# Performance work log

Hardware: AMD Instinct MI355X
Metric: run time of the kernel (lower is better)

Reference implementation:

```python
import jax, jax.numpy as jnp
import numpy as np

N_NODES = 50000
IN_NF = 64
HID = 128
OUT_NF = 64
EDGE_HID = HID // 2  # edge_nf_ratio = 2
N_LAYERS = 4
N_EDGES = 800000
NUM_LATENT_NODES = 64
C_EVEN = 1.0
C_ODD = 2.0 / NUM_LATENT_NODES


def setup_inputs() -> dict:
    key = jax.random.key(0)
    ks = jax.random.split(key, 24)
    def lin(k, fan_in, fan_out):
        # torch nn.Linear default init: U(-1/sqrt(fan_in), 1/sqrt(fan_in))
        bound = 1.0 / np.sqrt(fan_in)
        kw, kb = jax.random.split(k)
        w = jax.random.uniform(kw, (fan_in, fan_out), jnp.float32, -bound, bound)
        b = jax.random.uniform(kb, (fan_out,), jnp.float32, -bound, bound)
        return w, b

    h = jax.random.normal(ks[0], (N_NODES, IN_NF), jnp.float32)
    edges_a = jax.random.randint(ks[1], (2, N_EDGES), 0, N_NODES, jnp.int32)
    edges_b = jax.random.randint(ks[2], (2, N_EDGES), 0, N_NODES, jnp.int32)
    update_mask_a = jax.random.randint(ks[3], (N_NODES, 1), 0, 2, jnp.int32).astype(bool)
    update_mask_b = jax.random.randint(ks[4], (N_NODES, 1), 0, 2, jnp.int32).astype(bool)

    emb_in_w, emb_in_b = lin(ks[5], IN_NF, HID)
    emb_out_w, emb_out_b = lin(ks[6], HID, OUT_NF)

    ew1, eb1, ew2, eb2 = [], [], [], []
    nw1, nb1, nw2, nb2 = [], [], [], []
    for i in range(N_LAYERS):
        w, b = lin(ks[7 + i], 2 * HID, EDGE_HID); ew1.append(w); eb1.append(b)
        w, b = lin(ks[11 + i], EDGE_HID, EDGE_HID); ew2.append(w); eb2.append(b)
        w, b = lin(ks[15 + i], HID + EDGE_HID, HID); nw1.append(w); nb1.append(b)
        w, b = lin(ks[19 + i], HID, HID); nw2.append(w); nb2.append(b)

    stack = lambda xs: jnp.stack(xs, 0)
    return {
        "h": h, "edges_a": edges_a, "edges_b": edges_b,
        "update_mask_a": update_mask_a, "update_mask_b": update_mask_b,
        "emb_in_w": emb_in_w, "emb_in_b": emb_in_b,
        "emb_out_w": emb_out_w, "emb_out_b": emb_out_b,
        "edge_w1": stack(ew1), "edge_b1": stack(eb1),
        "edge_w2": stack(ew2), "edge_b2": stack(eb2),
        "node_w1": stack(nw1), "node_b1": stack(nb1),
        "node_w2": stack(nw2), "node_b2": stack(nb2),
    }


def _gcl(h, edges, mask, C, ew1, eb1, ew2, eb2, nw1, nb1, nw2, nb2):
    row, col = edges[0], edges[1]
    # edge model: gather source/target node feats -> 2-layer SiLU MLP
    feat = jnp.concatenate([h[row], h[col]], axis=-1)      # [E, 2*HID]
    m = jax.nn.silu(feat @ ew1 + eb1)                      # [E, EDGE_HID]
    m = jax.nn.silu(m @ ew2 + eb2)                         # [E, EDGE_HID]
    # aggregate messages to receiving nodes (scatter-add), scaled by C
    agg = jax.ops.segment_sum(m, row, num_segments=h.shape[0]) * C
    # node model with residual
    upd = jax.nn.silu(jnp.concatenate([h, agg], axis=-1) @ nw1 + nb1) @ nw2 + nb2
    h_new = h + upd
    # masked asynchronous update: only nodes with mask=True are updated
    return jnp.where(mask, h_new, h)


def reference(h, edges_a, edges_b, update_mask_a, update_mask_b,
              emb_in_w, emb_in_b, emb_out_w, emb_out_b,
              edge_w1, edge_b1, edge_w2, edge_b2,
              node_w1, node_b1, node_w2, node_b2):
    h = h @ emb_in_w + emb_in_b
    for i in range(N_LAYERS):
        if i % 2 == 0:
            edges, mask, C = edges_a, update_mask_a, C_EVEN
        else:
            edges, mask, C = edges_b, update_mask_b, C_ODD
        h = _gcl(h, edges, mask, C,
                 edge_w1[i], edge_b1[i], edge_w2[i], edge_b2[i],
                 node_w1[i], node_b1[i], node_w2[i], node_b2[i])
    h = h @ emb_out_w + emb_out_b
    return h
```

## Files before the change

kernel.cpp:

```cpp
#include <hip/hip_runtime.h>
#include <cstdint>

typedef __bf16 bf16_t;
typedef bf16_t bf16x8 __attribute__((ext_vector_type(8)));
typedef float floatx4 __attribute__((ext_vector_type(4)));
typedef unsigned short ushort4v __attribute__((ext_vector_type(4)));

constexpr int N_NODES = 50000;
constexpr int N_EDGES = 800000;
constexpr int HID = 128;
constexpr int EH = 64;
constexpr int NCH = (N_NODES + 255) / 256;

__device__ __forceinline__ float silu_f(float x) {
    return x * __builtin_amdgcn_rcpf(1.0f + __expf(-x));
}

__global__ __launch_bounds__(256) void pack_all_kernel(
    const float* __restrict__ embin, const float* __restrict__ embout,
    const float* __restrict__ ew1, const float* __restrict__ ew2,
    const float* __restrict__ nw1, const float* __restrict__ nw2,
    bf16_t* __restrict__ pk)
{
    int t = blockIdx.x * 256 + threadIdx.x;
    if (t >= 32768) {
        t -= 32768;
        int lane = t & 63, chunk = t >> 6;
        int ks = chunk & 3, nt = (chunk >> 2) & 7, l = chunk >> 5;
        int quad = lane >> 4, coln = lane & 15;
        const float* Wl = ew1 + l * 256 * 64;
        int kb = (nt >= 4 ? 128 : 0) + ks * 32 + quad * 8;
        int nc = (nt & 3) * 16 + coln;
        bf16x8 v;
#pragma unroll
        for (int j = 0; j < 8; j++) v[j] = (bf16_t)Wl[(kb + j) * 64 + nc];
        *(bf16x8*)(pk + 262144 + t * 8) = v;
        return;
    }
    const float* W; int K, Nc; int base; bf16_t* out;
    if (t < 1024)       { W = embin;  K = 64;  Nc = 128; base = 0;     out = pk; }
    else if (t < 2048)  { W = embout; K = 128; Nc = 64;  base = 1024;  out = pk + 8192; }
    else if (t < 10240) { W = ew1;    K = 256; Nc = 64;  base = 2048;  out = pk + 16384; }
    else if (t < 12288) { W = ew2;    K = 64;  Nc = 64;  base = 10240; out = pk + 81920; }
    else if (t < 24576) { W = nw1;    K = 192; Nc = 128; base = 12288; out = pk + 98304; }
    else                { W = nw2;    K = 128; Nc = 128; base = 24576; out = pk + 196608; }
    t -= base;
    int KS = K >> 5, NT = Nc >> 4;
    int lane = t & 63;
    int chunk = t >> 6;
    int ks = chunk % KS;
    int nt = (chunk / KS) % NT;
    int l  = chunk / (KS * NT);
    int quad = lane >> 4, coln = lane & 15;
    const float* Wl = W + l * K * Nc;
    bf16x8 v;
#pragma unroll
    for (int j = 0; j < 8; j++)
        v[j] = (bf16_t)Wl[(ks * 32 + quad * 8 + j) * Nc + nt * 16 + coln];
    *(bf16x8*)(out + t * 8) = v;
}

__global__ void hist2_kernel(const int* __restrict__ ea, const int* __restrict__ eb,
                             const int* __restrict__ ma, const int* __restrict__ mb,
                             int* __restrict__ ba, int* __restrict__ bb) {
    int half = gridDim.x >> 1;
    int b = blockIdx.x;
    const int* erows; const int* mask; int* bins;
    if (b < half) { erows = ea; mask = ma; bins = ba; }
    else          { erows = eb; mask = mb; bins = bb; b -= half; }
    int i = b * 256 + threadIdx.x;
    if (i >= N_EDGES) return;
    int r = erows[i];
    if (mask[r] != 0) atomicAdd(&bins[r], 1);
}

__global__ __launch_bounds__(256) void scan_phase1(
    const int* __restrict__ bins_a, const int* __restrict__ bins_b,
    int* __restrict__ bs_a, int* __restrict__ bs_b) {
    const int* bins = blockIdx.y ? bins_b : bins_a;
    int* bs = blockIdx.y ? bs_b : bs_a;
    int i = blockIdx.x * 256 + threadIdx.x;
    int v = (i < N_NODES) ? (bins[i] != 0 ? bins[i] : 0) : 0;
#pragma unroll
    for (int off = 32; off; off >>= 1) v += __shfl_down(v, off, 64);
    __shared__ int ws_[4];
    int lane = threadIdx.x & 63, wv = threadIdx.x >> 6;
    if (lane == 0) ws_[wv] = v;
    __syncthreads();
    if (threadIdx.x == 0) bs[blockIdx.x] = ws_[0] + ws_[1] + ws_[2] + ws_[3];
}

__global__ __launch_bounds__(256) void scan_phase2(
    int* __restrict__ bs_a, int* __restrict__ bs_b,
    int* __restrict__ bins_a, int* __restrict__ bins_b) {
    int* bs = blockIdx.x ? bs_b : bs_a;
    int* bins = blockIdx.x ? bins_b : bins_a;
    int t = threadIdx.x, lane = t & 63, wv = t >> 6;
    int v = (t < NCH) ? bs[t] : 0;
    int s = v;
#pragma unroll
    for (int off = 1; off < 64; off <<= 1) {
        int u = __shfl_up(s, off, 64);
        if (lane >= off) s += u;
    }
    __shared__ int wsum[4];
    if (lane == 63) wsum[wv] = s;
    __syncthreads();
    int woff = 0;
    for (int w = 0; w < wv; w++) woff += wsum[w];
    int excl = s - v + woff;
    if (t < NCH) bs[t] = excl;
    if (t == NCH - 1) bins[N_NODES] = excl + v;
}

__global__ __launch_bounds__(256) void mask_scan2(
    int* __restrict__ ms_a, int* __restrict__ ms_b,
    int* __restrict__ cnt_a, int* __restrict__ cnt_b) {
    int* ms = blockIdx.x ? ms_b : ms_a;
    int* cnt = blockIdx.x ? cnt_b : cnt_a;
    int t = threadIdx.x, lane = t & 63, wv = t >> 6;
    int v = (t < NCH) ? ms[t] : 0;
    int s = v;
#pragma unroll
    for (int off = 1; off < 64; off <<= 1) {
        int u = __shfl_up(s, off, 64);
        if (lane >= off) s += u;
    }
    __shared__ int wsum[4];
    if (lane == 63) wsum[wv] = s;
    __syncthreads();
    int woff = 0;
    for (int w = 0; w < wv; w++) woff += wsum[w];
    int excl = s - v + woff;
    if (t < NCH) ms[t] = excl;
    if (t == NCH - 1) cnt[0] = excl + v;
}

__global__ __launch_bounds__(256) void compact_kernel(
    const int* __restrict__ ma, const int* __restrict__ mb,
    const int* __restrict__ ms_a, const int* __restrict__ ms_b,
    int* __restrict__ la, int* __restrict__ lb) {
    const int* mask = blockIdx.y ? mb : ma;
    const int* ms = blockIdx.y ? ms_b : ms_a;
    int* list = blockIdx.y ? lb : la;
    int i = blockIdx.x * 256 + threadIdx.x;
    int t = threadIdx.x, lane = t & 63, wv = t >> 6;
    int m = (i < N_NODES) ? (mask[i] != 0) : 0;
    unsigned long long bal = __ballot(m != 0);
    int pos = (int)__popcll(bal & ((1ull << lane) - 1ull));
    __shared__ int wsum[4];
    if (lane == 63) wsum[wv] = pos + m;
    __syncthreads();
    int woff = 0;
    for (int w = 0; w < wv; w++) woff += wsum[w];
    if (m) list[ms[blockIdx.x] + woff + pos] = i;
}

__global__ __launch_bounds__(256) void scan_phase3(
    int* __restrict__ bins_a, int* __restrict__ bins_b,
    const int* __restrict__ bs_a, const int* __restrict__ bs_b) {
    int* bins = blockIdx.y ? bins_b : bins_a;
    const int* bs = blockIdx.y ? bs_b : bs_a;
    int i = blockIdx.x * 256 + threadIdx.x;
    int t = threadIdx.x, lane = t & 63, wv = t >> 6;
    int v = (i < N_NODES) ? bins[i] : 0;
    int s = v;
#pragma unroll
    for (int off = 1; off < 64; off <<= 1) {
        int u = __shfl_up(s, off, 64);
        if (lane >= off) s += u;
    }
    __shared__ int wsum[4];
    if (lane == 63) wsum[wv] = s;
    __syncthreads();
    int woff = 0;
    for (int w = 0; w < wv; w++) woff += wsum[w];
    if (i < N_NODES) bins[i] = s - v + woff + bs[blockIdx.x];
}

__global__ void fill_src_kernel(const int* __restrict__ bins_a, const int* __restrict__ bins_b,
                                int* __restrict__ ssrc_a, int* __restrict__ ssrc_b) {
    const int* bins = blockIdx.y ? bins_b : bins_a;
    int* ssrc = blockIdx.y ? ssrc_b : ssrc_a;
    int r = blockIdx.x * 256 + threadIdx.x;
    if (r >= N_NODES) return;
    int p0 = bins[r], p1 = bins[r + 1];
    for (int p = p0; p < p1; p++) ssrc[p] = r;
}

__global__ void scatter2_kernel(const int* __restrict__ ea, const int* __restrict__ eb,
                                const int* __restrict__ ma, const int* __restrict__ mb,
                                int* __restrict__ ba, int* __restrict__ bb,
                                int* __restrict__ sdst_a, int* __restrict__ sdst_b) {
    int half = gridDim.x >> 1;
    int b = blockIdx.x;
    const int* e; const int* mask; int* bins; int* sdst;
    if (b < half) { e = ea; mask = ma; bins = ba; sdst = sdst_a; }
    else          { e = eb; mask = mb; bins = bb; sdst = sdst_b; b -= half; }
    int i = b * 256 + threadIdx.x;
    if (i >= N_EDGES) return;
    int r = e[i];
    if (mask[r] == 0) return;
    int c = e[N_EDGES + i];
    int pos = atomicAdd(&bins[r], 1);
    sdst[pos] = c;
}

__global__ __launch_bounds__(256) void emb_in_kernel(
    const float* __restrict__ h0, const bf16_t* __restrict__ wp,
    const float* __restrict__ bias, float* __restrict__ h, bf16_t* __restrict__ h_bf)
{
    int t = threadIdx.x, wave = t >> 6, lane = t & 63;
    int quad = lane >> 4, col = lane & 15;
    int m0 = blockIdx.x * 64 + wave * 16;
    int ndc = min(m0 + col, N_NODES - 1);
    floatx4 acc[8] = {};
#pragma unroll
    for (int ks = 0; ks < 2; ks++) {
        const float* ap = h0 + ndc * 64 + ks * 32 + quad * 8;
        floatx4 f0 = *(const floatx4*)ap;
        floatx4 f1 = *(const floatx4*)(ap + 4);
        bf16x8 a;
#pragma unroll
        for (int j = 0; j < 4; j++) { a[j] = (bf16_t)f0[j]; a[j + 4] = (bf16_t)f1[j]; }
#pragma unroll
        for (int nt = 0; nt < 8; nt++) {
            bf16x8 b = ((const bf16x8*)wp)[(nt * 2 + ks) * 64 + lane];
            acc[nt] = __builtin_amdgcn_mfma_f32_16x16x32_bf16(a, b, acc[nt], 0, 0, 0);
        }
    }
#pragma unroll
    for (int r = 0; r < 4; r++) {
        int nd2 = m0 + quad * 4 + r;
        if (nd2 < N_NODES) {
#pragma unroll
            for (int nt = 0; nt < 8; nt++) {
                int n = nt * 16 + col;
                float x = acc[nt][r] + bias[n];
                h[nd2 * HID + n] = x;
                h_bf[nd2 * HID + n] = (bf16_t)x;
            }
        }
    }
}

__global__ __launch_bounds__(256) void pre_edge_kernel(
    const bf16_t* __restrict__ h_bf, const bf16_t* __restrict__ w1cat,
    const float* __restrict__ b1, float* __restrict__ P)
{
    int t = threadIdx.x, wave = t >> 6, lane = t & 63;
    int quad = lane >> 4, col = lane & 15;
    int m0 = blockIdx.x * 64 + wave * 16;
    int ndc = min(m0 + col, N_NODES - 1);
    floatx4 acc[8] = {};
#pragma unroll
    for (int ks = 0; ks < 4; ks++) {
        bf16x8 a = *(const bf16x8*)(h_bf + ndc * HID + ks * 32 + quad * 8);
#pragma unroll
        for (int nt = 0; nt < 8; nt++) {
            bf16x8 b = ((const bf16x8*)w1cat)[(nt * 4 + ks) * 64 + lane];
            acc[nt] = __builtin_amdgcn_mfma_f32_16x16x32_bf16(a, b, acc[nt], 0, 0, 0);
        }
    }
#pragma unroll
    for (int r = 0; r < 4; r++) {
        int nd2 = m0 + quad * 4 + r;
        if (nd2 < N_NODES) {
#pragma unroll
            for (int nt = 0; nt < 8; nt++) {
                int n = nt * 16 + col;
                float x = acc[nt][r] + (nt >= 4 ? b1[n - 64] : 0.0f);
                P[nd2 * 128 + n] = x;
            }
        }
    }
}

__global__ __launch_bounds__(256, 4) void edge_kernel_pre(
    const float* __restrict__ P, const int* __restrict__ ssrc,
    const int* __restrict__ sdst, const int* __restrict__ m_ptr,
    const bf16_t* __restrict__ w2p, const float* __restrict__ b2,
    float* __restrict__ agg, float C)
{
    __shared__ __align__(16) bf16_t pool[4][64 * 40];

    int t = threadIdx.x;
    int wave = t >> 6, lane = t & 63, quad = lane >> 4, col = lane & 15;
    bf16_t* mbT = pool[wave];

    float b2v[4];
#pragma unroll
    for (int nt = 0; nt < 4; nt++) b2v[nt] = b2[nt * 16 + col];

    int M = m_ptr[0];
    int ntiles = (M + 31) >> 5;
    int wid = blockIdx.x * 4 + wave, nw = gridDim.x * 4;
    if (wid >= ntiles) return;

    int sr = 0x7fffffff, ds = 0x7fffffff;
    { int p = wid * 32 + lane; if (lane < 32 && p < M) { sr = ssrc[p]; ds = sdst[p]; } }

    for (int tile = wid; tile < ntiles; tile += nw) {
        int tnc = min(tile + nw, ntiles - 1);
        int srn = 0x7fffffff, dsn = 0x7fffffff;
        { int p = tnc * 32 + lane; if (lane < 32 && p < M) { srn = ssrc[p]; dsn = sdst[p]; } }

        floatx4 acc2[2][4] = {};
#pragma unroll
        for (int m = 0; m < 2; m++) {
            int rN = min(__shfl(sr, m * 16 + col, 64), N_NODES - 1);
            int cN = min(__shfl(ds, m * 16 + col, 64), N_NODES - 1);
            const float* pr = P + rN * 128 + quad * 8;
            const float* pc = P + cN * 128 + 64 + quad * 8;
            floatx4 fr[4], fc[4];
#pragma unroll
            for (int ks = 0; ks < 2; ks++) {
                fr[ks * 2]     = *(const floatx4*)(pr + ks * 32);
                fr[ks * 2 + 1] = *(const floatx4*)(pr + ks * 32 + 4);
                fc[ks * 2]     = *(const floatx4*)(pc + ks * 32);
                fc[ks * 2 + 1] = *(const floatx4*)(pc + ks * 32 + 4);
            }
#pragma unroll
            for (int ks = 0; ks < 2; ks++) {
                bf16x8 a2;
#pragma unroll
                for (int j = 0; j < 4; j++) {
                    a2[j]     = (bf16_t)silu_f(fr[ks * 2][j]     + fc[ks * 2][j]);
                    a2[j + 4] = (bf16_t)silu_f(fr[ks * 2 + 1][j] + fc[ks * 2 + 1][j]);
                }
#pragma unroll
                for (int nt = 0; nt < 4; nt++) {
                    bf16x8 b = ((const bf16x8*)w2p)[(nt * 2 + ks) * 64 + lane];
                    acc2[m][nt] = __builtin_amdgcn_mfma_f32_16x16x32_bf16(a2, b, acc2[m][nt], 0, 0, 0);
                }
            }
        }

#pragma unroll
        for (int m = 0; m < 2; m++)
#pragma unroll
            for (int nt = 0; nt < 4; nt++) {
                ushort4v pv;
#pragma unroll
                for (int r = 0; r < 4; r++) {
                    bf16_t bv = (bf16_t)(silu_f(acc2[m][nt][r] + b2v[nt]) * C);
                    pv[r] = __builtin_bit_cast(unsigned short, bv);
                }
                *(ushort4v*)(mbT + (nt * 16 + col) * 40 + m * 16 + quad * 4) = pv;
            }

        {
            float mv[32];
#pragma unroll
            for (int i = 0; i < 4; i++) {
                bf16x8 v8 = *(const bf16x8*)(mbT + lane * 40 + i * 8);
#pragma unroll
                for (int j = 0; j < 8; j++) mv[i * 8 + j] = (float)v8[j];
            }
            int dp = __shfl(sr, 0, 64);
            float run = mv[0];
#pragma unroll
            for (int r = 1; r < 32; r++) {
                int d = __shfl(sr, r, 64);
                if (d != dp) {
                    if (dp < N_NODES) atomicAdd(agg + dp * EH + lane, run);
                    run = mv[r]; dp = d;
                } else run += mv[r];
            }
            if (dp < N_NODES) atomicAdd(agg + dp * EH + lane, run);
        }

        sr = srn; ds = dsn;
    }
}

__global__ __launch_bounds__(256, 3) void edge_kernel_sorted(
    const bf16_t* __restrict__ h_bf, const int* __restrict__ ssrc,
    const int* __restrict__ sdst, const int* __restrict__ m_ptr,
    const bf16_t* __restrict__ w1p, const float* __restrict__ b1,
    const bf16_t* __restrict__ w2p, const float* __restrict__ b2,
    float* __restrict__ agg, float C)
{
    __shared__ __align__(16) bf16_t w1s[16384];
    __shared__ __align__(16) bf16_t pool[4][64 * 40];

    int t = threadIdx.x;
#pragma unroll
    for (int i = 0; i < 8; i++)
        ((bf16x8*)w1s)[t + 256 * i] = ((const bf16x8*)w1p)[t + 256 * i];
    __syncthreads();

    int wave = t >> 6, lane = t & 63, quad = lane >> 4, col = lane & 15;
    bf16_t* hl = pool[wave];
    bf16_t* mbT = pool[wave];

    float b1v[4], b2v[4];
#pragma unroll
    for (int nt = 0; nt < 4; nt++) { b1v[nt] = b1[nt * 16 + col]; b2v[nt] = b2[nt * 16 + col]; }

    int M = m_ptr[0];
    int ntiles = (M + 31) >> 5;
    int wid = blockIdx.x * 4 + wave, nw = gridDim.x * 4;
    if (wid >= ntiles) return;

    int sr = 0x7fffffff, ds = 0x7fffffff;
    { int p = wid * 32 + lane; if (lane < 32 && p < M) { sr = ssrc[p]; ds = sdst[p]; } }
    bf16x8 a[2][8];
    {
        int ns0 = min(__shfl(sr, col, 64), N_NODES - 1);
        int ns1 = min(__shfl(sr, 16 + col, 64), N_NODES - 1);
        int nd0 = min(__shfl(ds, col, 64), N_NODES - 1);
        int nd1 = min(__shfl(ds, 16 + col, 64), N_NODES - 1);
#pragma unroll
        for (int ks = 0; ks < 8; ks++) {
            int o = (ks & 3) * 32 + quad * 8;
            a[0][ks] = *(const bf16x8*)(h_bf + (ks < 4 ? ns0 : nd0) * HID + o);
            a[1][ks] = *(const bf16x8*)(h_bf + (ks < 4 ? ns1 : nd1) * HID + o);
        }
    }

    for (int tile = wid; tile < ntiles; tile += nw) {
        int tnc = min(tile + nw, ntiles - 1);
        int srn = 0x7fffffff, dsn = 0x7fffffff;
        { int p = tnc * 32 + lane; if (lane < 32 && p < M) { srn = ssrc[p]; dsn = sdst[p]; } }

        floatx4 acc[2][4] = {};
#pragma unroll
        for (int ks = 0; ks < 8; ks++) {
#pragma unroll
            for (int nt = 0; nt < 4; nt++) {
                bf16x8 b = ((const bf16x8*)w1s)[(nt * 8 + ks) * 64 + lane];
                acc[0][nt] = __builtin_amdgcn_mfma_f32_16x16x32_bf16(a[0][ks], b, acc[0][nt], 0, 0, 0);
                acc[1][nt] = __builtin_amdgcn_mfma_f32_16x16x32_bf16(a[1][ks], b, acc[1][nt], 0, 0, 0);
            }
        }

        bf16x8 an[2][8];
        {
            int ns0 = min(__shfl(srn, col, 64), N_NODES - 1);
            int ns1 = min(__shfl(srn, 16 + col, 64), N_NODES - 1);
            int nd0 = min(__shfl(dsn, col, 64), N_NODES - 1);
            int nd1 = min(__shfl(dsn, 16 + col, 64), N_NODES - 1);
#pragma unroll
            for (int ks = 0; ks < 8; ks++) {
                int o = (ks & 3) * 32 + quad * 8;
                an[0][ks] = *(const bf16x8*)(h_bf + (ks < 4 ? ns0 : nd0) * HID + o);
                an[1][ks] = *(const bf16x8*)(h_bf + (ks < 4 ? ns1 : nd1) * HID + o);
            }
        }

#pragma unroll
        for (int m = 0; m < 2; m++)
#pragma unroll
            for (int nt = 0; nt < 4; nt++)
#pragma unroll
                for (int r = 0; r < 4; r++)
                    hl[(m * 16 + quad * 4 + r) * 72 + nt * 16 + col] =
                        (bf16_t)silu_f(acc[m][nt][r] + b1v[nt]);

        floatx4 acc2[2][4] = {};
#pragma unroll
        for (int ks = 0; ks < 2; ks++) {
            bf16x8 a2[2];
#pragma unroll
            for (int m = 0; m < 2; m++)
                a2[m] = *(const bf16x8*)(hl + (m * 16 + col) * 72 + ks * 32 + quad * 8);
#pragma unroll
            for (int nt = 0; nt < 4; nt++) {
                bf16x8 b = ((const bf16x8*)w2p)[(nt * 2 + ks) * 64 + lane];
                acc2[0][nt] = __builtin_amdgcn_mfma_f32_16x16x32_bf16(a2[0], b, acc2[0][nt], 0, 0, 0);
                acc2[1][nt] = __builtin_amdgcn_mfma_f32_16x16x32_bf16(a2[1], b, acc2[1][nt], 0, 0, 0);
            }
        }
#pragma unroll
        for (int m = 0; m < 2; m++)
#pragma unroll
            for (int nt = 0; nt < 4; nt++) {
                ushort4v p;
#pragma unroll
                for (int r = 0; r < 4; r++) {
                    bf16_t bv = (bf16_t)(silu_f(acc2[m][nt][r] + b2v[nt]) * C);
                    p[r] = __builtin_bit_cast(unsigned short, bv);
                }
                *(ushort4v*)(mbT + (nt * 16 + col) * 40 + m * 16 + quad * 4) = p;
            }

        {
            float mv[32];
#pragma unroll
            for (int i = 0; i < 4; i++) {
                bf16x8 v8 = *(const bf16x8*)(mbT + lane * 40 + i * 8);
#pragma unroll
                for (int j = 0; j < 8; j++) mv[i * 8 + j] = (float)v8[j];
            }
            int dp = __shfl(sr, 0, 64);
            float run = mv[0];
#pragma unroll
            for (int r = 1; r < 32; r++) {
                int d = __shfl(sr, r, 64);
                if (d != dp) {
                    if (dp < N_NODES) atomicAdd(agg + dp * EH + lane, run);
                    run = mv[r]; dp = d;
                } else run += mv[r];
            }
            if (dp < N_NODES) atomicAdd(agg + dp * EH + lane, run);
        }

        sr = srn; ds = dsn;
#pragma unroll
        for (int m = 0; m < 2; m++)
#pragma unroll
            for (int ks = 0; ks < 8; ks++) a[m][ks] = an[m][ks];
    }
}

__global__ __launch_bounds__(256) void edge_kernel(
    const bf16_t* __restrict__ h_bf, const int* __restrict__ edges,
    const int* __restrict__ mask,
    const bf16_t* __restrict__ w1p, const float* __restrict__ b1,
    const bf16_t* __restrict__ w2p, const float* __restrict__ b2,
    float* __restrict__ agg, float C)
{
    __shared__ __align__(16) bf16_t w1s[16384];
    __shared__ __align__(16) bf16_t w2s[4096];
    __shared__ __align__(16) bf16_t hl[4][16 * 72];

    int t = threadIdx.x;
#pragma unroll
    for (int i = 0; i < 8; i++)
        ((bf16x8*)w1s)[t + 256 * i] = ((const bf16x8*)w1p)[t + 256 * i];
#pragma unroll
    for (int i = 0; i < 2; i++)
        ((bf16x8*)w2s)[t + 256 * i] = ((const bf16x8*)w2p)[t + 256 * i];
    __syncthreads();

    int wave = t >> 6, lane = t & 63, quad = lane >> 4, col = lane & 15;
    bf16_t* myhl = hl[wave];

    float b1v[4], b2v[4];
#pragma unroll
    for (int nt = 0; nt < 4; nt++) { b1v[nt] = b1[nt * 16 + col]; b2v[nt] = b2[nt * 16 + col]; }

    const int ntile_cnt = N_EDGES / 64;
    for (int tile = blockIdx.x; tile < ntile_cnt; tile += gridDim.x) {
        int ebase = tile * 64 + wave * 16;
        int src = edges[ebase + col];
        int dst = edges[N_EDGES + ebase + col];

        floatx4 acc[4] = {};
#pragma unroll
        for (int ks = 0; ks < 8; ks++) {
            int idx = (ks < 4) ? src : dst;
            bf16x8 a = *(const bf16x8*)(h_bf + idx * HID + (ks & 3) * 32 + quad * 8);
#pragma unroll
            for (int nt = 0; nt < 4; nt++) {
                bf16x8 b = ((const bf16x8*)w1s)[(nt * 8 + ks) * 64 + lane];
                acc[nt] = __builtin_amdgcn_mfma_f32_16x16x32_bf16(a, b, acc[nt], 0, 0, 0);
            }
        }
#pragma unroll
        for (int nt = 0; nt < 4; nt++)
#pragma unroll
            for (int r = 0; r < 4; r++)
                myhl[(quad * 4 + r) * 72 + nt * 16 + col] = (bf16_t)silu_f(acc[nt][r] + b1v[nt]);
        __syncthreads();

        floatx4 acc2[4] = {};
#pragma unroll
        for (int ks = 0; ks < 2; ks++) {
            bf16x8 a = *(const bf16x8*)(myhl + col * 72 + ks * 32 + quad * 8);
#pragma unroll
            for (int nt = 0; nt < 4; nt++) {
                bf16x8 b = ((const bf16x8*)w2s)[(nt * 2 + ks) * 64 + lane];
                acc2[nt] = __builtin_amdgcn_mfma_f32_16x16x32_bf16(a, b, acc2[nt], 0, 0, 0);
            }
        }
#pragma unroll
        for (int r = 0; r < 4; r++) {
            int dest = edges[ebase + quad * 4 + r];
            if (mask[dest] != 0) {
                float* aggp = agg + dest * EH;
#pragma unroll
                for (int nt = 0; nt < 4; nt++) {
                    float x = acc2[nt][r] + b2v[nt];
                    atomicAdd(aggp + nt * 16 + col, silu_f(x) * C);
                }
            }
        }
        __syncthreads();
    }
}

__global__ __launch_bounds__(256) void node_kernel_masked(
    float* __restrict__ h, bf16_t* __restrict__ h_bf,
    float* __restrict__ agg, const int* __restrict__ list,
    const int* __restrict__ cnt_ptr,
    const bf16_t* __restrict__ w1p, const float* __restrict__ b1,
    const bf16_t* __restrict__ w2p, const float* __restrict__ b2)
{
    __shared__ __align__(16) bf16_t hl[4][16 * 136];
    int t = threadIdx.x, wave = t >> 6, lane = t & 63;
    int quad = lane >> 4, col = lane & 15;
    int cnt = cnt_ptr[0];
    int m0 = blockIdx.x * 64 + wave * 16;
    if (m0 >= cnt) return;
    int lv = list[min(m0 + col, cnt - 1)];
    int ndc = lv;

    floatx4 acc[8] = {};
#pragma unroll
    for (int ks = 0; ks < 6; ks++) {
        bf16x8 a;
        if (ks < 4) {
            a = *(const bf16x8*)(h_bf + ndc * HID + ks * 32 + quad * 8);
        } else {
            const float* ap = agg + ndc * EH + (ks - 4) * 32 + quad * 8;
            floatx4 f0 = *(const floatx4*)ap;
            floatx4 f1 = *(const floatx4*)(ap + 4);
#pragma unroll
            for (int j = 0; j < 4; j++) { a[j] = (bf16_t)f0[j]; a[j + 4] = (bf16_t)f1[j]; }
        }
#pragma unroll
        for (int nt = 0; nt < 8; nt++) {
            bf16x8 b = ((const bf16x8*)w1p)[(nt * 6 + ks) * 64 + lane];
            acc[nt] = __builtin_amdgcn_mfma_f32_16x16x32_bf16(a, b, acc[nt], 0, 0, 0);
        }
    }
    if ((m0 + col) < cnt) {
        floatx4 z = {0.0f, 0.0f, 0.0f, 0.0f};
        float* zp = agg + ndc * EH + quad * 8;
        *(floatx4*)zp = z; *(floatx4*)(zp + 4) = z;
        *(floatx4*)(zp + 32) = z; *(floatx4*)(zp + 36) = z;
    }
    bf16_t* myhl = hl[wave];
#pragma unroll
    for (int nt = 0; nt < 8; nt++)
#pragma unroll
        for (int r = 0; r < 4; r++) {
            float x = acc[nt][r] + b1[nt * 16 + col];
            myhl[(quad * 4 + r) * 136 + nt * 16 + col] = (bf16_t)silu_f(x);
        }

    floatx4 acc2[8] = {};
#pragma unroll
    for (int ks = 0; ks < 4; ks++) {
        bf16x8 a = *(const bf16x8*)(myhl + col * 136 + ks * 32 + quad * 8);
#pragma unroll
        for (int nt = 0; nt < 8; nt++) {
            bf16x8 b = ((const bf16x8*)w2p)[(nt * 4 + ks) * 64 + lane];
            acc2[nt] = __builtin_amdgcn_mfma_f32_16x16x32_bf16(a, b, acc2[nt], 0, 0, 0);
        }
    }
#pragma unroll
    for (int r = 0; r < 4; r++) {
        if ((m0 + quad * 4 + r) < cnt) {
            int nd2 = __shfl(lv, quad * 4 + r, 64);
#pragma unroll
            for (int nt = 0; nt < 8; nt++) {
                int n = nt * 16 + col;
                float hv = h[nd2 * HID + n] + acc2[nt][r] + b2[n];
                h[nd2 * HID + n] = hv;
                h_bf[nd2 * HID + n] = (bf16_t)hv;
            }
        }
    }
}

__global__ __launch_bounds__(256) void node_kernel(
    float* __restrict__ h, bf16_t* __restrict__ h_bf,
    float* __restrict__ agg, const int* __restrict__ mask,
    const bf16_t* __restrict__ w1p, const float* __restrict__ b1,
    const bf16_t* __restrict__ w2p, const float* __restrict__ b2,
    const bf16_t* __restrict__ wop, const float* __restrict__ bo,
    float* __restrict__ out)
{
    __shared__ __align__(16) bf16_t hl[4][16 * 136];
    int t = threadIdx.x, wave = t >> 6, lane = t & 63;
    int quad = lane >> 4, col = lane & 15;
    int m0 = blockIdx.x * 64 + wave * 16;
    int ndc = min(m0 + col, N_NODES - 1);

    floatx4 acc[8] = {};
#pragma unroll
    for (int ks = 0; ks < 6; ks++) {
        bf16x8 a;
        if (ks < 4) {
            a = *(const bf16x8*)(h_bf + ndc * HID + ks * 32 + quad * 8);
        } else {
            const float* ap = agg + ndc * EH + (ks - 4) * 32 + quad * 8;
            floatx4 f0 = *(const floatx4*)ap;
            floatx4 f1 = *(const floatx4*)(ap + 4);
#pragma unroll
            for (int j = 0; j < 4; j++) { a[j] = (bf16_t)f0[j]; a[j + 4] = (bf16_t)f1[j]; }
        }
#pragma unroll
        for (int nt = 0; nt < 8; nt++) {
            bf16x8 b = ((const bf16x8*)w1p)[(nt * 6 + ks) * 64 + lane];
            acc[nt] = __builtin_amdgcn_mfma_f32_16x16x32_bf16(a, b, acc[nt], 0, 0, 0);
        }
    }
    bf16_t* myhl = hl[wave];
#pragma unroll
    for (int nt = 0; nt < 8; nt++)
#pragma unroll
        for (int r = 0; r < 4; r++) {
            float x = acc[nt][r] + b1[nt * 16 + col];
            myhl[(quad * 4 + r) * 136 + nt * 16 + col] = (bf16_t)silu_f(x);
        }

    floatx4 acc2[8] = {};
#pragma unroll
    for (int ks = 0; ks < 4; ks++) {
        bf16x8 a = *(const bf16x8*)(myhl + col * 136 + ks * 32 + quad * 8);
#pragma unroll
        for (int nt = 0; nt < 8; nt++) {
            bf16x8 b = ((const bf16x8*)w2p)[(nt * 4 + ks) * 64 + lane];
            acc2[nt] = __builtin_amdgcn_mfma_f32_16x16x32_bf16(a, b, acc2[nt], 0, 0, 0);
        }
    }
#pragma unroll
    for (int r = 0; r < 4; r++) {
        int nd2 = m0 + quad * 4 + r;
        bool valid = nd2 < N_NODES;
        bool upd = valid && mask[min(nd2, N_NODES - 1)] != 0;
        if (upd) {
#pragma unroll
            for (int nt = 0; nt < 8; nt++) {
                int n = nt * 16 + col;
                float hv = h[nd2 * HID + n] + acc2[nt][r] + b2[n];
                h[nd2 * HID + n] = hv;
                bf16_t hb = (bf16_t)hv;
                h_bf[nd2 * HID + n] = hb;
                myhl[(quad * 4 + r) * 136 + n] = hb;
            }
        } else {
#pragma unroll
            for (int nt = 0; nt < 8; nt++) {
                int n = nt * 16 + col;
                myhl[(quad * 4 + r) * 136 + n] =
                    valid ? h_bf[nd2 * HID + n] : (bf16_t)0.0f;
            }
        }
    }
    floatx4 ao[4] = {};
#pragma unroll
    for (int ks = 0; ks < 4; ks++) {
        bf16x8 a = *(const bf16x8*)(myhl + col * 136 + ks * 32 + quad * 8);
#pragma unroll
        for (int nt = 0; nt < 4; nt++) {
            bf16x8 b = ((const bf16x8*)wop)[(nt * 4 + ks) * 64 + lane];
            ao[nt] = __builtin_amdgcn_mfma_f32_16x16x32_bf16(a, b, ao[nt], 0, 0, 0);
        }
    }
#pragma unroll
    for (int r = 0; r < 4; r++) {
        int nd2 = m0 + quad * 4 + r;
        if (nd2 < N_NODES) {
#pragma unroll
            for (int nt = 0; nt < 4; nt++) {
                int n = nt * 16 + col;
                out[nd2 * 64 + n] = ao[nt][r] + bo[n];
            }
        }
    }
}

extern "C" void kernel_launch(void* const* d_in, const int* in_sizes, int n_in,
                              void* d_out, int out_size, void* d_ws, size_t ws_size,
                              hipStream_t stream) {
    const float* h0        = (const float*)d_in[0];
    const int*   edges_a   = (const int*)d_in[1];
    const int*   edges_b   = (const int*)d_in[2];
    const int*   mask_a    = (const int*)d_in[3];
    const int*   mask_b    = (const int*)d_in[4];
    const float* emb_in_w  = (const float*)d_in[5];
    const float* emb_in_b  = (const float*)d_in[6];
    const float* emb_out_w = (const float*)d_in[7];
    const float* emb_out_b = (const float*)d_in[8];
    const float* ew1 = (const float*)d_in[9];
    const float* eb1 = (const float*)d_in[10];
    const float* ew2 = (const float*)d_in[11];
    const float* eb2 = (const float*)d_in[12];
    const float* nw1 = (const float*)d_in[13];
    const float* nb1 = (const float*)d_in[14];
    const float* nw2 = (const float*)d_in[15];
    const float* nb2 = (const float*)d_in[16];

    const size_t SZ_H = 25600000, SZ_HBF = 12800000, SZ_AGG = 12800000;
    const size_t SZ_PK = 655360;
    const size_t SZ_S = 3200000, SZ_BINS = 200704, SZ_BS = 1024, SZ_LIST = 200704;
    const size_t SZ_P = 25600000;

    char* ws = (char*)d_ws;
    size_t off = 0;
    float*  h    = (float*)(ws + off);  off += SZ_H;
    bf16_t* h_bf = (bf16_t*)(ws + off); off += SZ_HBF;
    float*  agg  = (float*)(ws + off);  off += SZ_AGG;
    bf16_t* pk   = (bf16_t*)(ws + off); off += SZ_PK;
    int* ssrc_a = (int*)(ws + off); off += SZ_S;
    int* sdst_a = (int*)(ws + off); off += SZ_S;
    int* ssrc_b = (int*)(ws + off); off += SZ_S;
    int* sdst_b = (int*)(ws + off); off += SZ_S;
    int* bins_a = (int*)(ws + off); off += SZ_BINS;
    int* bins_b = (int*)(ws + off); off += SZ_BINS;
    int* bs_a   = (int*)(ws + off); off += SZ_BS;
    int* bs_b   = (int*)(ws + off); off += SZ_BS;
    int* ms_a   = (int*)(ws + off); off += SZ_BS;
    int* ms_b   = (int*)(ws + off); off += SZ_BS;
    int* cnt_a  = (int*)(ws + off); off += 256;
    int* cnt_b  = (int*)(ws + off); off += 256;
    int* list_a = (int*)(ws + off); off += SZ_LIST;
    int* list_b = (int*)(ws + off); off += SZ_LIST;
    bool sorted_path = (ws_size >= off);
    float* P = (float*)(ws + off); off += SZ_P;
    bool pre_path = (ws_size >= off);

    bf16_t* pk_embin  = pk;
    bf16_t* pk_embout = pk + 8192;
    bf16_t* pk_ew1    = pk + 16384;
    bf16_t* pk_ew2    = pk + 81920;
    bf16_t* pk_nw1    = pk + 98304;
    bf16_t* pk_nw2    = pk + 196608;
    bf16_t* pk_ew1cat = pk + 262144;

    pack_all_kernel<<<160, 256, 0, stream>>>(emb_in_w, emb_out_w, ew1, ew2, nw1, nw2, pk);

    const int edge_grid = (N_EDGES + 255) / 256;
    const int node_blocks = (N_NODES + 63) / 64;
    if (sorted_path) {
        hipMemsetAsync(bins_a, 0, 2 * SZ_BINS + 2 * SZ_BS, stream);
        hist2_kernel<<<2 * edge_grid, 256, 0, stream>>>(edges_a, edges_b, mask_a, mask_b,
                                                        bins_a, bins_b);
        scan_phase1<<<dim3(NCH, 2), 256, 0, stream>>>(bins_a, bins_b, bs_a, bs_b);
        scan_phase2<<<2, 256, 0, stream>>>(bs_a, bs_b, bins_a, bins_b);
        scan_phase3<<<dim3(NCH, 2), 256, 0, stream>>>(bins_a, bins_b, bs_a, bs_b);
        fill_src_kernel<<<dim3(NCH, 2), 256, 0, stream>>>(bins_a, bins_b, ssrc_a, ssrc_b);
        scatter2_kernel<<<2 * edge_grid, 256, 0, stream>>>(edges_a, edges_b, mask_a, mask_b,
                                                           bins_a, bins_b, sdst_a, sdst_b);
        scan_phase1<<<dim3(NCH, 2), 256, 0, stream>>>(mask_a, mask_b, ms_a, ms_b);
        mask_scan2<<<2, 256, 0, stream>>>(ms_a, ms_b, cnt_a, cnt_b);
        compact_kernel<<<dim3(NCH, 2), 256, 0, stream>>>(mask_a, mask_b, ms_a, ms_b,
                                                         list_a, list_b);
    }

    hipMemsetAsync(agg, 0, (size_t)N_NODES * EH * 4, stream);
    emb_in_kernel<<<node_blocks, 256, 0, stream>>>(h0, pk_embin, emb_in_b, h, h_bf);

    for (int l = 0; l < 4; l++) {
        const int* mask = (l & 1) ? mask_b : mask_a;
        float C = (l & 1) ? 0.03125f : 1.0f;
        if (pre_path) {
            const int* ssrc = (l & 1) ? ssrc_b : ssrc_a;
            const int* sdst = (l & 1) ? sdst_b : sdst_a;
            const int* mp   = ((l & 1) ? bins_b : bins_a) + N_NODES;
            pre_edge_kernel<<<node_blocks, 256, 0, stream>>>(
                h_bf, pk_ew1cat + l * 16384, eb1 + l * 64, P);
            edge_kernel_pre<<<1024, 256, 0, stream>>>(P, ssrc, sdst, mp,
                                                      pk_ew2 + l * 4096, eb2 + l * 64,
                                                      agg, C);
        } else if (sorted_path) {
            const int* ssrc = (l & 1) ? ssrc_b : ssrc_a;
            const int* sdst = (l & 1) ? sdst_b : sdst_a;
            const int* mp   = ((l & 1) ? bins_b : bins_a) + N_NODES;
            edge_kernel_sorted<<<768, 256, 0, stream>>>(h_bf, ssrc, sdst, mp,
                                                        pk_ew1 + l * 16384, eb1 + l * 64,
                                                        pk_ew2 + l * 4096,  eb2 + l * 64,
                                                        agg, C);
        } else {
            const int* edges = (l & 1) ? edges_b : edges_a;
            edge_kernel<<<768, 256, 0, stream>>>(h_bf, edges, mask,
                                                 pk_ew1 + l * 16384, eb1 + l * 64,
                                                 pk_ew2 + l * 4096,  eb2 + l * 64,
                                                 agg, C);
        }
        if (l < 3 && sorted_path) {
            const int* list = (l & 1) ? list_b : list_a;
            const int* cnt  = (l & 1) ? cnt_b : cnt_a;
            node_kernel_masked<<<node_blocks, 256, 0, stream>>>(
                h, h_bf, agg, list, cnt,
                pk_nw1 + l * 24576, nb1 + l * 128,
                pk_nw2 + l * 16384, nb2 + l * 128);
        } else if (l < 3) {
            node_kernel<<<node_blocks, 256, 0, stream>>>(h, h_bf, agg, mask,
                                                         pk_nw1 + l * 24576, nb1 + l * 128,
                                                         pk_nw2 + l * 16384, nb2 + l * 128,
                                                         pk_embout, emb_out_b, (float*)d_out);
            hipMemsetAsync(agg, 0, (size_t)N_NODES * EH * 4, stream);
        } else {
            node_kernel<<<node_blocks, 256, 0, stream>>>(h, h_bf, agg, mask,
                                                         pk_nw1 + 3 * 24576, nb1 + 3 * 128,
                                                         pk_nw2 + 3 * 16384, nb2 + 3 * 128,
                                                         pk_embout, emb_out_b, (float*)d_out);
        }
    }
}
```

Baseline: 439.8 us.

## Fuse setup kernels, embedding with layer-0 projection, and prefetch edge gathers

Several things change at once. The scan-phase3 and fill-source kernels are merged into one kernel, and the embedding kernel now also computes layer 0's per-node edge projection P, so layer 0 no longer launches pre_edge_kernel. The agg buffer is moved next to bins so a single memset clears both, replacing a separate memset. The edge kernel software-prefetches the next tile's P rows into registers while the current tile computes, and its occupancy hint and grid size are lowered to leave room for the extra registers. The aim is fewer launches and hidden gather latency, at the cost of more register pressure and lower occupancy.

```diff
diff --git a/kernel.cpp b/kernel.cpp
--- a/kernel.cpp
+++ b/kernel.cpp
@@ -156,11 +156,13 @@
     if (m) list[ms[blockIdx.x] + woff + pos] = i;
 }
 
-__global__ __launch_bounds__(256) void scan_phase3(
+__global__ __launch_bounds__(256) void scan3_fill(
     int* __restrict__ bins_a, int* __restrict__ bins_b,
-    const int* __restrict__ bs_a, const int* __restrict__ bs_b) {
+    const int* __restrict__ bs_a, const int* __restrict__ bs_b,
+    int* __restrict__ ssrc_a, int* __restrict__ ssrc_b) {
     int* bins = blockIdx.y ? bins_b : bins_a;
     const int* bs = blockIdx.y ? bs_b : bs_a;
+    int* ssrc = blockIdx.y ? ssrc_b : ssrc_a;
     int i = blockIdx.x * 256 + threadIdx.x;
     int t = threadIdx.x, lane = t & 63, wv = t >> 6;
     int v = (i < N_NODES) ? bins[i] : 0;
@@ -175,17 +177,11 @@
     __syncthreads();
     int woff = 0;
     for (int w = 0; w < wv; w++) woff += wsum[w];
-    if (i < N_NODES) bins[i] = s - v + woff + bs[blockIdx.x];
-}
-
-__global__ void fill_src_kernel(const int* __restrict__ bins_a, const int* __restrict__ bins_b,
-                                int* __restrict__ ssrc_a, int* __restrict__ ssrc_b) {
-    const int* bins = blockIdx.y ? bins_b : bins_a;
-    int* ssrc = blockIdx.y ? ssrc_b : ssrc_a;
-    int r = blockIdx.x * 256 + threadIdx.x;
-    if (r >= N_NODES) return;
-    int p0 = bins[r], p1 = bins[r + 1];
-    for (int p = p0; p < p1; p++) ssrc[p] = r;
+    if (i < N_NODES) {
+        int p0 = s - v + woff + bs[blockIdx.x];
+        bins[i] = p0;
+        for (int p = p0; p < p0 + v; p++) ssrc[p] = i;
+    }
 }
 
 __global__ void scatter2_kernel(const int* __restrict__ ea, const int* __restrict__ eb,
@@ -244,6 +240,74 @@
     }
 }
 
+__global__ __launch_bounds__(256) void emb_in_p0_kernel(
+    const float* __restrict__ h0, const bf16_t* __restrict__ wp,
+    const float* __restrict__ bias, float* __restrict__ h, bf16_t* __restrict__ h_bf,
+    const bf16_t* __restrict__ w1cat, const float* __restrict__ b1,
+    float* __restrict__ P)
+{
+    __shared__ __align__(16) bf16_t hl[4][16 * 136];
+    int t = threadIdx.x, wave = t >> 6, lane = t & 63;
+    int quad = lane >> 4, col = lane & 15;
+    int m0 = blockIdx.x * 64 + wave * 16;
+    int ndc = min(m0 + col, N_NODES - 1);
+    floatx4 acc[8] = {};
+#pragma unroll
+    for (int ks = 0; ks < 2; ks++) {
+        const float* ap = h0 + ndc * 64 + ks * 32 + quad * 8;
+        floatx4 f0 = *(const floatx4*)ap;
+        floatx4 f1 = *(const floatx4*)(ap + 4);
+        bf16x8 a;
+#pragma unroll
+        for (int j = 0; j < 4; j++) { a[j] = (bf16_t)f0[j]; a[j + 4] = (bf16_t)f1[j]; }
+#pragma unroll
+        for (int nt = 0; nt < 8; nt++) {
+            bf16x8 b = ((const bf16x8*)wp)[(nt * 2 + ks) * 64 + lane];
+            acc[nt] = __builtin_amdgcn_mfma_f32_16x16x32_bf16(a, b, acc[nt], 0, 0, 0);
+        }
+    }
+    bf16_t* myhl = hl[wave];
+#pragma unroll
+    for (int r = 0; r < 4; r++) {
+        int nd2 = m0 + quad * 4 + r;
+        bool valid = nd2 < N_NODES;
+#pragma unroll
+        for (int nt = 0; nt < 8; nt++) {
+            int n = nt * 16 + col;
+            if (valid) {
+                float x = acc[nt][r] + bias[n];
+                h[nd2 * HID + n] = x;
+                bf16_t hb = (bf16_t)x;
+                h_bf[nd2 * HID + n] = hb;
+                myhl[(quad * 4 + r) * 136 + n] = hb;
+            } else {
+                myhl[(quad * 4 + r) * 136 + n] = (bf16_t)0.0f;
+            }
+        }
+    }
+    floatx4 accp[8] = {};
+#pragma unroll
+    for (int ks = 0; ks < 4; ks++) {
+        bf16x8 a = *(const bf16x8*)(myhl + col * 136 + ks * 32 + quad * 8);
+#pragma unroll
+        for (int nt = 0; nt < 8; nt++) {
+            bf16x8 b = ((const bf16x8*)w1cat)[(nt * 4 + ks) * 64 + lane];
+            accp[nt] = __builtin_amdgcn_mfma_f32_16x16x32_bf16(a, b, accp[nt], 0, 0, 0);
+        }
+    }
+#pragma unroll
+    for (int r = 0; r < 4; r++) {
+        int nd2 = m0 + quad * 4 + r;
+        if (nd2 < N_NODES) {
+#pragma unroll
+            for (int nt = 0; nt < 8; nt++) {
+                int n = nt * 16 + col;
+                P[nd2 * 128 + n] = accp[nt][r] + (nt >= 4 ? b1[n - 64] : 0.0f);
+            }
+        }
+    }
+}
+
 __global__ __launch_bounds__(256) void pre_edge_kernel(
     const bf16_t* __restrict__ h_bf, const bf16_t* __restrict__ w1cat,
     const float* __restrict__ b1, float* __restrict__ P)
@@ -276,7 +340,7 @@
     }
 }
 
-__global__ __launch_bounds__(256, 4) void edge_kernel_pre(
+__global__ __launch_bounds__(256, 3) void edge_kernel_pre(
     const float* __restrict__ P, const int* __restrict__ ssrc,
     const int* __restrict__ sdst, const int* __restrict__ m_ptr,
     const bf16_t* __restrict__ w2p, const float* __restrict__ b2,
@@ -300,6 +364,19 @@
     int sr = 0x7fffffff, ds = 0x7fffffff;
     { int p = wid * 32 + lane; if (lane < 32 && p < M) { sr = ssrc[p]; ds = sdst[p]; } }
 
+    floatx4 frp[2][4], fcp[2][4];
+#pragma unroll
+    for (int m = 0; m < 2; m++) {
+        int rN = min(__shfl(sr, m * 16 + col, 64), N_NODES - 1);
+        int cN = min(__shfl(ds, m * 16 + col, 64), N_NODES - 1);
+        const float* pr = P + rN * 128 + quad * 8;
+        const float* pc = P + cN * 128 + 64 + quad * 8;
+        frp[m][0] = *(const floatx4*)pr;        frp[m][1] = *(const floatx4*)(pr + 4);
+        frp[m][2] = *(const floatx4*)(pr + 32); frp[m][3] = *(const floatx4*)(pr + 36);
+        fcp[m][0] = *(const floatx4*)pc;        fcp[m][1] = *(const floatx4*)(pc + 4);
+        fcp[m][2] = *(const floatx4*)(pc + 32); fcp[m][3] = *(const floatx4*)(pc + 36);
+    }
+
     for (int tile = wid; tile < ntiles; tile += nw) {
         int tnc = min(tile + nw, ntiles - 1);
         int srn = 0x7fffffff, dsn = 0x7fffffff;
@@ -308,25 +385,13 @@
         floatx4 acc2[2][4] = {};
 #pragma unroll
         for (int m = 0; m < 2; m++) {
-            int rN = min(__shfl(sr, m * 16 + col, 64), N_NODES - 1);
-            int cN = min(__shfl(ds, m * 16 + col, 64), N_NODES - 1);
-            const float* pr = P + rN * 128 + quad * 8;
-            const float* pc = P + cN * 128 + 64 + quad * 8;
-            floatx4 fr[4], fc[4];
-#pragma unroll
-            for (int ks = 0; ks < 2; ks++) {
-                fr[ks * 2]     = *(const floatx4*)(pr + ks * 32);
-                fr[ks * 2 + 1] = *(const floatx4*)(pr + ks * 32 + 4);
-                fc[ks * 2]     = *(const floatx4*)(pc + ks * 32);
-                fc[ks * 2 + 1] = *(const floatx4*)(pc + ks * 32 + 4);
-            }
 #pragma unroll
             for (int ks = 0; ks < 2; ks++) {
                 bf16x8 a2;
 #pragma unroll
                 for (int j = 0; j < 4; j++) {
-                    a2[j]     = (bf16_t)silu_f(fr[ks * 2][j]     + fc[ks * 2][j]);
-                    a2[j + 4] = (bf16_t)silu_f(fr[ks * 2 + 1][j] + fc[ks * 2 + 1][j]);
+                    a2[j]     = (bf16_t)silu_f(frp[m][ks * 2][j]     + fcp[m][ks * 2][j]);
+                    a2[j + 4] = (bf16_t)silu_f(frp[m][ks * 2 + 1][j] + fcp[m][ks * 2 + 1][j]);
                 }
 #pragma unroll
                 for (int nt = 0; nt < 4; nt++) {
@@ -334,6 +399,19 @@
                     acc2[m][nt] = __builtin_amdgcn_mfma_f32_16x16x32_bf16(a2, b, acc2[m][nt], 0, 0, 0);
                 }
             }
+        }
+
+        floatx4 frn[2][4], fcn[2][4];
+#pragma unroll
+        for (int m = 0; m < 2; m++) {
+            int rN = min(__shfl(srn, m * 16 + col, 64), N_NODES - 1);
+            int cN = min(__shfl(dsn, m * 16 + col, 64), N_NODES - 1);
+            const float* pr = P + rN * 128 + quad * 8;
+            const float* pc = P + cN * 128 + 64 + quad * 8;
+            frn[m][0] = *(const floatx4*)pr;        frn[m][1] = *(const floatx4*)(pr + 4);
+            frn[m][2] = *(const floatx4*)(pr + 32); frn[m][3] = *(const floatx4*)(pr + 36);
+            fcn[m][0] = *(const floatx4*)pc;        fcn[m][1] = *(const floatx4*)(pc + 4);
+            fcn[m][2] = *(const floatx4*)(pc + 32); fcn[m][3] = *(const floatx4*)(pc + 36);
         }
 
 #pragma unroll
@@ -371,6 +449,10 @@
         }
 
         sr = srn; ds = dsn;
+#pragma unroll
+        for (int m = 0; m < 2; m++)
+#pragma unroll
+            for (int k = 0; k < 4; k++) { frp[m][k] = frn[m][k]; fcp[m][k] = fcn[m][k]; }
     }
 }
 
@@ -795,7 +877,6 @@
     size_t off = 0;
     float*  h    = (float*)(ws + off);  off += SZ_H;
     bf16_t* h_bf = (bf16_t*)(ws + off); off += SZ_HBF;
-    float*  agg  = (float*)(ws + off);  off += SZ_AGG;
     bf16_t* pk   = (bf16_t*)(ws + off); off += SZ_PK;
     int* ssrc_a = (int*)(ws + off); off += SZ_S;
     int* sdst_a = (int*)(ws + off); off += SZ_S;
@@ -803,6 +884,7 @@
     int* sdst_b = (int*)(ws + off); off += SZ_S;
     int* bins_a = (int*)(ws + off); off += SZ_BINS;
     int* bins_b = (int*)(ws + off); off += SZ_BINS;
+    float* agg  = (float*)(ws + off); off += SZ_AGG;
     int* bs_a   = (int*)(ws + off); off += SZ_BS;
     int* bs_b   = (int*)(ws + off); off += SZ_BS;
     int* ms_a   = (int*)(ws + off); off += SZ_BS;
@@ -828,23 +910,29 @@
     const int edge_grid = (N_EDGES + 255) / 256;
     const int node_blocks = (N_NODES + 63) / 64;
     if (sorted_path) {
-        hipMemsetAsync(bins_a, 0, 2 * SZ_BINS + 2 * SZ_BS, stream);
+        hipMemsetAsync(bins_a, 0, 2 * SZ_BINS + SZ_AGG, stream);
         hist2_kernel<<<2 * edge_grid, 256, 0, stream>>>(edges_a, edges_b, mask_a, mask_b,
                                                         bins_a, bins_b);
         scan_phase1<<<dim3(NCH, 2), 256, 0, stream>>>(bins_a, bins_b, bs_a, bs_b);
         scan_phase2<<<2, 256, 0, stream>>>(bs_a, bs_b, bins_a, bins_b);
-        scan_phase3<<<dim3(NCH, 2), 256, 0, stream>>>(bins_a, bins_b, bs_a, bs_b);
-        fill_src_kernel<<<dim3(NCH, 2), 256, 0, stream>>>(bins_a, bins_b, ssrc_a, ssrc_b);
+        scan3_fill<<<dim3(NCH, 2), 256, 0, stream>>>(bins_a, bins_b, bs_a, bs_b,
+                                                     ssrc_a, ssrc_b);
         scatter2_kernel<<<2 * edge_grid, 256, 0, stream>>>(edges_a, edges_b, mask_a, mask_b,
                                                            bins_a, bins_b, sdst_a, sdst_b);
         scan_phase1<<<dim3(NCH, 2), 256, 0, stream>>>(mask_a, mask_b, ms_a, ms_b);
         mask_scan2<<<2, 256, 0, stream>>>(ms_a, ms_b, cnt_a, cnt_b);
         compact_kernel<<<dim3(NCH, 2), 256, 0, stream>>>(mask_a, mask_b, ms_a, ms_b,
                                                          list_a, list_b);
-    }
-
-    hipMemsetAsync(agg, 0, (size_t)N_NODES * EH * 4, stream);
-    emb_in_kernel<<<node_blocks, 256, 0, stream>>>(h0, pk_embin, emb_in_b, h, h_bf);
+    } else {
+        hipMemsetAsync(agg, 0, SZ_AGG, stream);
+    }
+
+    if (pre_path) {
+        emb_in_p0_kernel<<<node_blocks, 256, 0, stream>>>(
+            h0, pk_embin, emb_in_b, h, h_bf, pk_ew1cat, eb1, P);
+    } else {
+        emb_in_kernel<<<node_blocks, 256, 0, stream>>>(h0, pk_embin, emb_in_b, h, h_bf);
+    }
 
     for (int l = 0; l < 4; l++) {
         const int* mask = (l & 1) ? mask_b : mask_a;
@@ -853,11 +941,12 @@
             const int* ssrc = (l & 1) ? ssrc_b : ssrc_a;
             const int* sdst = (l & 1) ? sdst_b : sdst_a;
             const int* mp   = ((l & 1) ? bins_b : bins_a) + N_NODES;
-            pre_edge_kernel<<<node_blocks, 256, 0, stream>>>(
-                h_bf, pk_ew1cat + l * 16384, eb1 + l * 64, P);
-            edge_kernel_pre<<<1024, 256, 0, stream>>>(P, ssrc, sdst, mp,
-                                                      pk_ew2 + l * 4096, eb2 + l * 64,
-                                                      agg, C);
+            if (l > 0)
+                pre_edge_kernel<<<node_blocks, 256, 0, stream>>>(
+                    h_bf, pk_ew1cat + l * 16384, eb1 + l * 64, P);
+            edge_kernel_pre<<<768, 256, 0, stream>>>(P, ssrc, sdst, mp,
+                                                     pk_ew2 + l * 4096, eb2 + l * 64,
+                                                     agg, C);
         } else if (sorted_path) {
             const int* ssrc = (l & 1) ? ssrc_b : ssrc_a;
             const int* sdst = (l & 1) ? sdst_b : sdst_a;
@@ -885,7 +974,7 @@
                                                          pk_nw1 + l * 24576, nb1 + l * 128,
                                                          pk_nw2 + l * 16384, nb2 + l * 128,
                                                          pk_embout, emb_out_b, (float*)d_out);
-            hipMemsetAsync(agg, 0, (size_t)N_NODES * EH * 4, stream);
+            hipMemsetAsync(agg, 0, SZ_AGG, stream);
         } else {
             node_kernel<<<node_blocks, 256, 0, stream>>>(h, h_bf, agg, mask,
                                                          pk_nw1 + 3 * 24576, nb1 + 3 * 128,
```

New measurement: 450.9 us. 2.5% more time.
